# Kernel optimization log

Measured on AMD Instinct MI355X. Metric: run time of the kernel, lower is better.

The kernel has to match this reference:

```python
import jax, jax.numpy as jnp
import numpy as np

N_EMBD = 1024
D_FF = 4 * N_EMBD
RANK = 4
NUM_LOOPS = 4
SCALE = 1.0 / RANK  # alpha=1.0 / r=4


def setup_inputs() -> dict:
    key = jax.random.key(0)
    ks = jax.random.split(key, 8)
    B, T = 8, 2048
    x = jax.random.normal(ks[0], (B, T, N_EMBD), dtype=jnp.float32)
    # base linears (torch nn.Linear weight layout: [out, in]), bias=False
    W1 = jax.random.normal(ks[1], (D_FF, N_EMBD), dtype=jnp.float32) * (1.0 / np.sqrt(N_EMBD))
    W2 = jax.random.normal(ks[2], (N_EMBD, D_FF), dtype=jnp.float32) * (1.0 / np.sqrt(D_FF))
    # LoRA factors: A [num_loops, r, in], B [num_loops, out, r]
    # (torch inits lora_B to zeros; we use small random values so the LoRA path is exercised)
    A1 = jax.random.normal(ks[3], (NUM_LOOPS, RANK, N_EMBD), dtype=jnp.float32) * (1.0 / np.sqrt(N_EMBD))
    B1 = jax.random.normal(ks[4], (NUM_LOOPS, D_FF, RANK), dtype=jnp.float32) * 0.01
    A2 = jax.random.normal(ks[5], (NUM_LOOPS, RANK, D_FF), dtype=jnp.float32) * (1.0 / np.sqrt(D_FF))
    B2 = jax.random.normal(ks[6], (NUM_LOOPS, N_EMBD, RANK), dtype=jnp.float32) * 0.01
    adapter_id = 1
    return {"x": x, "W1": W1, "A1": A1, "B1": B1, "W2": W2, "A2": A2, "B2": B2,
            "adapter_id": adapter_id}


def _lora_linear(x, W, A, B, adapter_id):
    # base: x @ W.T  (torch F.linear)
    out = jnp.einsum('btd,fd->btf', x, W)
    Aa = A[adapter_id]  # [r, in]
    Ba = B[adapter_id]  # [out, r]
    # low-rank correction: ((x @ A.T) @ B.T) * scale
    delta = jnp.einsum('btr,fr->btf', jnp.einsum('btd,rd->btr', x, Aa), Ba) * SCALE
    return out + delta


def reference(x, W1, A1, B1, W2, A2, B2, adapter_id):
    h = jax.nn.relu(_lora_linear(x, W1, A1, B1, adapter_id))
    out = _lora_linear(h, W2, A2, B2, adapter_id)
    # Dropout in eval mode (identity); see notes.
    return out
```

## Files before the change

### kernel.cpp

```cpp
#include <hip/hip_runtime.h>
#include <stdint.h>

typedef __bf16 bf16;
typedef __attribute__((ext_vector_type(8))) __bf16 bf16x8;
typedef __attribute__((ext_vector_type(4))) float f32x4;

#define LORA_SCALE 0.25f

__device__ __forceinline__ void gload_lds16(const bf16* g, bf16* l) {
    __builtin_amdgcn_global_load_lds(
        (const __attribute__((address_space(1))) uint32_t*)g,
        (__attribute__((address_space(3))) uint32_t*)l,
        16, 0, 0);
}

__device__ __forceinline__ bf16x8 cvt8(const float* p) {
    f32x4 a = *(const f32x4*)p;
    f32x4 b = *(const f32x4*)(p + 4);
    bf16x8 r;
    r[0] = (bf16)a[0]; r[1] = (bf16)a[1]; r[2] = (bf16)a[2]; r[3] = (bf16)a[3];
    r[4] = (bf16)b[0]; r[5] = (bf16)b[1]; r[6] = (bf16)b[2]; r[7] = (bf16)b[3];
    return r;
}

__global__ __launch_bounds__(256)
void cvt_f32_bf16(const float* __restrict__ in, bf16* __restrict__ out) {
    const int idx = (blockIdx.x * 256 + threadIdx.x) * 8;
    *(bf16x8*)&out[idx] = cvt8(&in[idx]);
}

__device__ __forceinline__ void ld8_f32(const bf16* p, float* o) {
    bf16x8 v = *(const bf16x8*)p;
    #pragma unroll
    for (int e = 0; e < 8; e++) o[e] = (float)v[e];
}
__device__ __forceinline__ void ld8_f32(const float* p, float* o) {
    f32x4 a = *(const f32x4*)p;
    f32x4 b = *(const f32x4*)(p + 4);
    o[0] = a[0]; o[1] = a[1]; o[2] = a[2]; o[3] = a[3];
    o[4] = b[0]; o[5] = b[1]; o[6] = b[2]; o[7] = b[3];
}

template<int K, typename XT, bool CVT>
__global__ __launch_bounds__(256)
void lora_down(const XT* __restrict__ X, const float* __restrict__ Aall,
               const int* __restrict__ adapter, float* __restrict__ T,
               bf16* __restrict__ Xb)
{
    const int aid = adapter[0];
    const float* Aa = Aall + (int64_t)aid * 4 * K;
    const int wid  = (blockIdx.x * 256 + threadIdx.x) >> 6;
    const int lane = threadIdx.x & 63;
    const XT* xr = X + (int64_t)wid * K;

    float a0 = 0.f, a1 = 0.f, a2 = 0.f, a3 = 0.f;
    #pragma unroll
    for (int it = 0; it < K / 512; it++) {
        const int k = it * 512 + lane * 8;
        float xv[8], r0[8], r1[8], r2[8], r3[8];
        ld8_f32(&xr[k], xv);
        ld8_f32(&Aa[0 * K + k], r0);
        ld8_f32(&Aa[1 * K + k], r1);
        ld8_f32(&Aa[2 * K + k], r2);
        ld8_f32(&Aa[3 * K + k], r3);
        if (CVT) {
            bf16x8 xb;
            #pragma unroll
            for (int e = 0; e < 8; e++) xb[e] = (bf16)xv[e];
            *(bf16x8*)&Xb[(int64_t)wid * K + k] = xb;
        }
        #pragma unroll
        for (int e = 0; e < 8; e++) {
            a0 += xv[e] * r0[e];
            a1 += xv[e] * r1[e];
            a2 += xv[e] * r2[e];
            a3 += xv[e] * r3[e];
        }
    }
    #pragma unroll
    for (int off = 32; off >= 1; off >>= 1) {
        a0 += __shfl_xor(a0, off);
        a1 += __shfl_xor(a1, off);
        a2 += __shfl_xor(a2, off);
        a3 += __shfl_xor(a3, off);
    }
    if (lane == 0) {
        f32x4 t;
        t[0] = a0; t[1] = a1; t[2] = a2; t[3] = a3;
        *(f32x4*)&T[(int64_t)wid * 4] = t;
    }
}

template<bool RELU, typename CT>
__global__ __launch_bounds__(256, 2)
void gemm_lora(const bf16* __restrict__ A,
               const bf16* __restrict__ Bm,
               CT* __restrict__ C,
               const float* __restrict__ Tlo,
               const float* __restrict__ Blo,
               const int* __restrict__ adapter,
               int M, int N, int K)
{
    __shared__ bf16 smem[256 * 64 + 128 * 64];
    bf16* sA = smem;
    bf16* sB = smem + 256 * 64;

    const int tid  = threadIdx.x;
    const int lane = tid & 63;
    const int w    = tid >> 6;
    const int quad = lane >> 4;
    const int l16  = lane & 15;

    const int nBase = blockIdx.x * 128;
    const int mBase = blockIdx.y * 256;
    const int wm = (w >> 1) * 128;
    const int wn = (w & 1) * 64;

    f32x4 acc[8][4];
    #pragma unroll
    for (int i = 0; i < 8; i++)
        #pragma unroll
        for (int j = 0; j < 4; j++)
            #pragma unroll
            for (int e = 0; e < 4; e++)
                acc[i][j][e] = 0.f;

    const bf16* gA = A  + (int64_t)mBase * K;
    const bf16* gB = Bm + (int64_t)nBase * K;
    const int ldRow  = tid >> 3;
    const int swzCol = ((tid & 7) ^ ((tid >> 3) & 7)) * 8;

    for (int kt = 0; kt < K; kt += 64) {
        #pragma unroll
        for (int i = 0; i < 8; i++)
            gload_lds16(gA + (int64_t)(i * 32 + ldRow) * K + kt + swzCol,
                        sA + (i * 32 + w * 8) * 64);
        #pragma unroll
        for (int i = 0; i < 4; i++)
            gload_lds16(gB + (int64_t)(i * 32 + ldRow) * K + kt + swzCol,
                        sB + (i * 32 + w * 8) * 64);
        __syncthreads();
        #pragma unroll
        for (int ks = 0; ks < 2; ks++) {
            const int kpos = (((ks * 4 + quad) ^ (l16 & 7))) * 8;
            bf16x8 af[8], bfv[4];
            #pragma unroll
            for (int i = 0; i < 8; i++)
                af[i] = *(const bf16x8*)&sA[(wm + i * 16 + l16) * 64 + kpos];
            #pragma unroll
            for (int j = 0; j < 4; j++)
                bfv[j] = *(const bf16x8*)&sB[(wn + j * 16 + l16) * 64 + kpos];
            #pragma unroll
            for (int i = 0; i < 8; i++)
                #pragma unroll
                for (int j = 0; j < 4; j++)
                    acc[i][j] = __builtin_amdgcn_mfma_f32_16x16x32_bf16(af[i], bfv[j], acc[i][j], 0, 0, 0);
        }
        __syncthreads();
    }

    const int aid = adapter[0];
    const float* Ba = Blo + (int64_t)aid * N * 4;

    f32x4 bv[4];
    #pragma unroll
    for (int j = 0; j < 4; j++) {
        const int f = nBase + wn + j * 16 + l16;
        bv[j] = *(const f32x4*)&Ba[(int64_t)f * 4];
    }

    if constexpr (sizeof(CT) == 2) {
        bf16* scratch = smem + w * (64 * 72);
        #pragma unroll
        for (int g = 0; g < 2; g++) {
            #pragma unroll
            for (int mi2 = 0; mi2 < 4; mi2++) {
                const int mi = g * 4 + mi2;
                f32x4 tv[4];
                #pragma unroll
                for (int r = 0; r < 4; r++) {
                    const int m = mBase + wm + mi * 16 + quad * 4 + r;
                    tv[r] = *(const f32x4*)&Tlo[(int64_t)m * 4];
                }
                #pragma unroll
                for (int j = 0; j < 4; j++) {
                    #pragma unroll
                    for (int r = 0; r < 4; r++) {
                        const float d = tv[r][0] * bv[j][0] + tv[r][1] * bv[j][1]
                                      + tv[r][2] * bv[j][2] + tv[r][3] * bv[j][3];
                        float v = acc[mi][j][r] + LORA_SCALE * d;
                        if (RELU) v = v > 0.f ? v : 0.f;
                        scratch[(mi2 * 16 + quad * 4 + r) * 72 + j * 16 + l16] = (bf16)v;
                    }
                }
            }
            #pragma unroll
            for (int p = 0; p < 8; p++) {
                const int row = p * 8 + (lane >> 3);
                bf16x8 vv = *(const bf16x8*)&scratch[row * 72 + (lane & 7) * 8];
                const int m = mBase + wm + g * 64 + row;
                *(bf16x8*)&C[(int64_t)m * N + nBase + wn + (lane & 7) * 8] = vv;
            }
        }
    } else {
        #pragma unroll
        for (int mi = 0; mi < 8; mi++) {
            f32x4 tv[4];
            #pragma unroll
            for (int r = 0; r < 4; r++) {
                const int m = mBase + wm + mi * 16 + quad * 4 + r;
                tv[r] = *(const f32x4*)&Tlo[(int64_t)m * 4];
            }
            #pragma unroll
            for (int j = 0; j < 4; j++) {
                #pragma unroll
                for (int r = 0; r < 4; r++) {
                    const float d = tv[r][0] * bv[j][0] + tv[r][1] * bv[j][1]
                                  + tv[r][2] * bv[j][2] + tv[r][3] * bv[j][3];
                    float v = acc[mi][j][r] + LORA_SCALE * d;
                    if (RELU) v = v > 0.f ? v : 0.f;
                    const int m = mBase + wm + mi * 16 + quad * 4 + r;
                    C[(int64_t)m * N + nBase + wn + j * 16 + l16] = v;
                }
            }
        }
    }
}

extern "C" void kernel_launch(void* const* d_in, const int* in_sizes, int n_in,
                              void* d_out, int out_size, void* d_ws, size_t ws_size,
                              hipStream_t stream) {
    const float* x  = (const float*)d_in[0];
    const float* W1 = (const float*)d_in[1];
    const float* A1 = (const float*)d_in[2];
    const float* B1 = (const float*)d_in[3];
    const float* W2 = (const float*)d_in[4];
    const float* A2 = (const float*)d_in[5];
    const float* B2 = (const float*)d_in[6];
    const int* adapter = (const int*)d_in[7];
    float* out = (float*)d_out;

    const int M = 16384, D = 1024, F = 4096;

    bf16*  h  = (bf16*)d_ws;
    bf16*  xb = h + (size_t)M * F;
    bf16*  wb = xb + (size_t)M * D;
    float* t1 = (float*)(wb + (size_t)F * D);
    float* t2 = t1 + (size_t)M * 4;

    lora_down<1024, float, true><<<M / 4, 256, 0, stream>>>(x, A1, adapter, t1, xb);
    cvt_f32_bf16<<<(F * D) / 2048, 256, 0, stream>>>(W1, wb);
    dim3 g1(F / 128, M / 256);
    gemm_lora<true, bf16><<<g1, 256, 0, stream>>>(xb, wb, h, t1, B1, adapter, M, F, D);
    lora_down<4096, bf16, false><<<M / 4, 256, 0, stream>>>(h, A2, adapter, t2, nullptr);
    cvt_f32_bf16<<<(D * F) / 2048, 256, 0, stream>>>(W2, wb);
    dim3 g2(D / 128, M / 256);
    gemm_lora<false, float><<<g2, 256, 0, stream>>>(h, wb, out, t2, B2, adapter, M, D, F);
}
```

Baseline: 486.2 us.

## Fuse second LoRA down-projection into first GEMM epilogue and remap blocks per XCD

The separate lora_down pass over h (M×4096 bf16) is removed. Its work moves into the first GEMM's epilogue, which dots each ReLU output tile with A2, reduces across the wave and atomically adds into T2. T2 is zeroed in the first LoRA kernel, which now handles 4 rows per wave. Blocks are remapped so tiles sharing operands land on the same XCD, and launch bounds are raised to 3 blocks per CU. This saves a full re-read of h, at the cost of many float atomics and a summation order that is no longer deterministic.

```diff
diff --git a/kernel.cpp b/kernel.cpp
--- a/kernel.cpp
+++ b/kernel.cpp
@@ -29,76 +29,85 @@
     *(bf16x8*)&out[idx] = cvt8(&in[idx]);
 }
 
-__device__ __forceinline__ void ld8_f32(const bf16* p, float* o) {
-    bf16x8 v = *(const bf16x8*)p;
-    #pragma unroll
-    for (int e = 0; e < 8; e++) o[e] = (float)v[e];
-}
-__device__ __forceinline__ void ld8_f32(const float* p, float* o) {
-    f32x4 a = *(const f32x4*)p;
-    f32x4 b = *(const f32x4*)(p + 4);
-    o[0] = a[0]; o[1] = a[1]; o[2] = a[2]; o[3] = a[3];
-    o[4] = b[0]; o[5] = b[1]; o[6] = b[2]; o[7] = b[3];
-}
-
-template<int K, typename XT, bool CVT>
 __global__ __launch_bounds__(256)
-void lora_down(const XT* __restrict__ X, const float* __restrict__ Aall,
-               const int* __restrict__ adapter, float* __restrict__ T,
-               bf16* __restrict__ Xb)
+void lora1(const float* __restrict__ X, const float* __restrict__ Aall,
+           const int* __restrict__ adapter, float* __restrict__ T,
+           bf16* __restrict__ Xb, float* __restrict__ T2, int M)
 {
+    const int K = 1024;
+    const int gid = blockIdx.x * 256 + threadIdx.x;
+    if (gid < M) {
+        f32x4 z; z[0] = 0.f; z[1] = 0.f; z[2] = 0.f; z[3] = 0.f;
+        *(f32x4*)&T2[(int64_t)gid * 4] = z;
+    }
+
     const int aid = adapter[0];
     const float* Aa = Aall + (int64_t)aid * 4 * K;
-    const int wid  = (blockIdx.x * 256 + threadIdx.x) >> 6;
+    const int wid  = gid >> 6;
     const int lane = threadIdx.x & 63;
-    const XT* xr = X + (int64_t)wid * K;
-
-    float a0 = 0.f, a1 = 0.f, a2 = 0.f, a3 = 0.f;
+    const int m0   = wid * 4;
+
+    float acc[4][4];
+    #pragma unroll
+    for (int rr = 0; rr < 4; rr++)
+        #pragma unroll
+        for (int r = 0; r < 4; r++) acc[rr][r] = 0.f;
+
     #pragma unroll
     for (int it = 0; it < K / 512; it++) {
         const int k = it * 512 + lane * 8;
-        float xv[8], r0[8], r1[8], r2[8], r3[8];
-        ld8_f32(&xr[k], xv);
-        ld8_f32(&Aa[0 * K + k], r0);
-        ld8_f32(&Aa[1 * K + k], r1);
-        ld8_f32(&Aa[2 * K + k], r2);
-        ld8_f32(&Aa[3 * K + k], r3);
-        if (CVT) {
+        float av[4][8];
+        #pragma unroll
+        for (int r = 0; r < 4; r++) {
+            f32x4 a = *(const f32x4*)&Aa[r * K + k];
+            f32x4 b = *(const f32x4*)&Aa[r * K + k + 4];
+            av[r][0]=a[0]; av[r][1]=a[1]; av[r][2]=a[2]; av[r][3]=a[3];
+            av[r][4]=b[0]; av[r][5]=b[1]; av[r][6]=b[2]; av[r][7]=b[3];
+        }
+        #pragma unroll
+        for (int rr = 0; rr < 4; rr++) {
+            const float* xp = X + (int64_t)(m0 + rr) * K + k;
+            f32x4 a = *(const f32x4*)xp;
+            f32x4 b = *(const f32x4*)(xp + 4);
+            float xv[8] = {a[0],a[1],a[2],a[3],b[0],b[1],b[2],b[3]};
             bf16x8 xb;
             #pragma unroll
             for (int e = 0; e < 8; e++) xb[e] = (bf16)xv[e];
-            *(bf16x8*)&Xb[(int64_t)wid * K + k] = xb;
-        }
-        #pragma unroll
-        for (int e = 0; e < 8; e++) {
-            a0 += xv[e] * r0[e];
-            a1 += xv[e] * r1[e];
-            a2 += xv[e] * r2[e];
-            a3 += xv[e] * r3[e];
-        }
-    }
-    #pragma unroll
-    for (int off = 32; off >= 1; off >>= 1) {
-        a0 += __shfl_xor(a0, off);
-        a1 += __shfl_xor(a1, off);
-        a2 += __shfl_xor(a2, off);
-        a3 += __shfl_xor(a3, off);
-    }
+            *(bf16x8*)&Xb[(int64_t)(m0 + rr) * K + k] = xb;
+            #pragma unroll
+            for (int r = 0; r < 4; r++)
+                #pragma unroll
+                for (int e = 0; e < 8; e++)
+                    acc[rr][r] += xv[e] * av[r][e];
+        }
+    }
+    #pragma unroll
+    for (int rr = 0; rr < 4; rr++)
+        #pragma unroll
+        for (int r = 0; r < 4; r++)
+            #pragma unroll
+            for (int off = 32; off >= 1; off >>= 1)
+                acc[rr][r] += __shfl_xor(acc[rr][r], off);
     if (lane == 0) {
-        f32x4 t;
-        t[0] = a0; t[1] = a1; t[2] = a2; t[3] = a3;
-        *(f32x4*)&T[(int64_t)wid * 4] = t;
-    }
-}
-
-template<bool RELU, typename CT>
-__global__ __launch_bounds__(256, 2)
+        #pragma unroll
+        for (int rr = 0; rr < 4; rr++) {
+            f32x4 t;
+            t[0] = acc[rr][0]; t[1] = acc[rr][1]; t[2] = acc[rr][2]; t[3] = acc[rr][3];
+            *(f32x4*)&T[(int64_t)(m0 + rr) * 4] = t;
+        }
+    }
+}
+
+template<bool RELU, typename CT, int PART, bool FUSET2>
+__global__ __launch_bounds__(256, 3)
 void gemm_lora(const bf16* __restrict__ A,
                const bf16* __restrict__ Bm,
                CT* __restrict__ C,
                const float* __restrict__ Tlo,
                const float* __restrict__ Blo,
                const int* __restrict__ adapter,
+               const float* __restrict__ A2,
+               float* __restrict__ T2,
                int M, int N, int K)
 {
     __shared__ bf16 smem[256 * 64 + 128 * 64];
@@ -111,8 +120,16 @@
     const int quad = lane >> 4;
     const int l16  = lane & 15;
 
-    const int nBase = blockIdx.x * 128;
-    const int mBase = blockIdx.y * 256;
+    int bx, by;
+    {
+        const int Nt = gridDim.x, Mt = gridDim.y;
+        const int id = blockIdx.y * Nt + blockIdx.x;
+        const int xcd = id & 7, k = id >> 3;
+        if (PART == 0) { const int q = Nt >> 3; bx = xcd * q + (k % q); by = k / q; }
+        else           { const int q = Mt >> 3; bx = k % Nt; by = xcd * q + (k / Nt); }
+    }
+    const int nBase = bx * 128;
+    const int mBase = by * 256;
     const int wm = (w >> 1) * 128;
     const int wn = (w & 1) * 64;
 
@@ -169,6 +186,18 @@
         bv[j] = *(const f32x4*)&Ba[(int64_t)f * 4];
     }
 
+    float a2v[4][4];
+    if (FUSET2) {
+        const float* A2a = A2 + (int64_t)aid * 4 * N;
+        #pragma unroll
+        for (int j = 0; j < 4; j++) {
+            const int f = nBase + wn + j * 16 + l16;
+            #pragma unroll
+            for (int r2 = 0; r2 < 4; r2++)
+                a2v[j][r2] = A2a[(int64_t)r2 * N + f];
+        }
+    }
+
     if constexpr (sizeof(CT) == 2) {
         bf16* scratch = smem + w * (64 * 72);
         #pragma unroll
@@ -182,6 +211,12 @@
                     const int m = mBase + wm + mi * 16 + quad * 4 + r;
                     tv[r] = *(const f32x4*)&Tlo[(int64_t)m * 4];
                 }
+                float tp[4][4];
+                if (FUSET2)
+                    #pragma unroll
+                    for (int r = 0; r < 4; r++)
+                        #pragma unroll
+                        for (int r2 = 0; r2 < 4; r2++) tp[r][r2] = 0.f;
                 #pragma unroll
                 for (int j = 0; j < 4; j++) {
                     #pragma unroll
@@ -190,7 +225,29 @@
                                       + tv[r][2] * bv[j][2] + tv[r][3] * bv[j][3];
                         float v = acc[mi][j][r] + LORA_SCALE * d;
                         if (RELU) v = v > 0.f ? v : 0.f;
+                        if (FUSET2)
+                            #pragma unroll
+                            for (int r2 = 0; r2 < 4; r2++)
+                                tp[r][r2] += v * a2v[j][r2];
                         scratch[(mi2 * 16 + quad * 4 + r) * 72 + j * 16 + l16] = (bf16)v;
+                    }
+                }
+                if (FUSET2) {
+                    #pragma unroll
+                    for (int r = 0; r < 4; r++)
+                        #pragma unroll
+                        for (int r2 = 0; r2 < 4; r2++)
+                            #pragma unroll
+                            for (int off = 8; off >= 1; off >>= 1)
+                                tp[r][r2] += __shfl_xor(tp[r][r2], off);
+                    if (l16 == 0) {
+                        #pragma unroll
+                        for (int r = 0; r < 4; r++) {
+                            const int m = mBase + wm + mi * 16 + quad * 4 + r;
+                            #pragma unroll
+                            for (int r2 = 0; r2 < 4; r2++)
+                                atomicAdd(&T2[(int64_t)m * 4 + r2], tp[r][r2]);
+                        }
                     }
                 }
             }
@@ -248,12 +305,13 @@
     float* t1 = (float*)(wb + (size_t)F * D);
     float* t2 = t1 + (size_t)M * 4;
 
-    lora_down<1024, float, true><<<M / 4, 256, 0, stream>>>(x, A1, adapter, t1, xb);
+    lora1<<<M / 16, 256, 0, stream>>>(x, A1, adapter, t1, xb, t2, M);
     cvt_f32_bf16<<<(F * D) / 2048, 256, 0, stream>>>(W1, wb);
     dim3 g1(F / 128, M / 256);
-    gemm_lora<true, bf16><<<g1, 256, 0, stream>>>(xb, wb, h, t1, B1, adapter, M, F, D);
-    lora_down<4096, bf16, false><<<M / 4, 256, 0, stream>>>(h, A2, adapter, t2, nullptr);
+    gemm_lora<true, bf16, 0, true><<<g1, 256, 0, stream>>>(
+        xb, wb, h, t1, B1, adapter, A2, t2, M, F, D);
     cvt_f32_bf16<<<(D * F) / 2048, 256, 0, stream>>>(W2, wb);
     dim3 g2(D / 128, M / 256);
-    gemm_lora<false, float><<<g2, 256, 0, stream>>>(h, wb, out, t2, B2, adapter, M, D, F);
-}
+    gemm_lora<false, float, 1, false><<<g2, 256, 0, stream>>>(
+        h, wb, out, t2, B2, adapter, nullptr, nullptr, M, D, F);
+}
```

Measured after the change: 895.9 us. 84.3% more time.
